# Optimization experiments

Measured on AMD Instinct MI355X. Metric: run time of the kernel, lower is better.

## Reference

```python
import jax, jax.numpy as jnp
import numpy as np

D_MODEL, D_STATE, V_RANGE, IMG, K = 64, 16, 1, 32, 3
GROUPS = 4
EPS = 1e-5


def _gather_indices():
    H = W = IMG
    v_list = [(x, y) for x in range(-V_RANGE, V_RANGE + 1) for y in range(-V_RANGE, V_RANGE + 1)]
    idx = []
    yg, xg = np.meshgrid(np.arange(H), np.arange(W), indexing='ij')
    for vx, vy in v_list:
        src_y = (yg - vy) % H
        src_x = (xg - vx) % W
        idx.append((src_y * W + src_x).reshape(-1))
    return jnp.asarray(np.stack(idx, axis=0), dtype=jnp.int32)  # (V, H*W)


def setup_inputs() -> dict:
    key = jax.random.key(0)
    ks = jax.random.split(key, 8)
    B = 4
    V = (2 * V_RANGE + 1) ** 2
    fan = D_MODEL * K * K
    std = 1.0 / np.sqrt(fan)
    return {
        'u_t': jax.random.normal(ks[0], (B, D_MODEL, IMG, IMG), jnp.float32),
        's_prev': jax.random.normal(ks[1], (B, V, D_MODEL, D_STATE, IMG, IMG), jnp.float32),
        'gamma': jnp.ones((D_MODEL,), jnp.float32),
        'beta': jnp.zeros((D_MODEL,), jnp.float32),
        'w_delta': jax.random.uniform(ks[2], (D_MODEL, D_MODEL, K, K), jnp.float32, -std, std),
        'b_delta': jax.random.uniform(ks[3], (D_MODEL,), jnp.float32, -std, std),
        'w_B': jax.random.uniform(ks[4], (D_STATE, D_MODEL, K, K), jnp.float32, -std, std),
        'w_C': jax.random.uniform(ks[5], (D_STATE, D_MODEL, K, K), jnp.float32, -std, std),
        'log_A_real': jnp.log(0.5 * jnp.ones((D_MODEL, D_STATE), jnp.float32)),
        'D_param': jnp.ones((D_MODEL,), jnp.float32),
        'dt_inv_softplus': jnp.asarray(np.log(np.exp(1.0) - 1.0), jnp.float32),
        'gather_indices': _gather_indices(),
    }


def _group_norm(x, gamma, beta):
    B, D, H, W = x.shape
    xg = x.reshape(B, GROUPS, D // GROUPS, H, W)
    mu = xg.mean(axis=(2, 3, 4), keepdims=True)
    var = xg.var(axis=(2, 3, 4), keepdims=True)
    xn = ((xg - mu) / jnp.sqrt(var + EPS)).reshape(B, D, H, W)
    return xn * gamma[None, :, None, None] + beta[None, :, None, None]


def _circ_conv(x, w, b=None):
    p = K // 2
    xp = jnp.pad(x, ((0, 0), (0, 0), (p, p), (p, p)), mode='wrap')
    y = jax.lax.conv_general_dilated(xp, w, (1, 1), 'VALID',
                                     dimension_numbers=('NCHW', 'OIHW', 'NCHW'))
    if b is not None:
        y = y + b[None, :, None, None]
    return y


def reference(u_t, s_prev, gamma, beta, w_delta, b_delta, w_B, w_C,
              log_A_real, D_param, dt_inv_softplus, gather_indices):
    B, D, H, W = u_t.shape
    Bv, V, _, N, _, _ = s_prev.shape
    u_norm = _group_norm(u_t, gamma, beta)
    delta = jax.nn.softplus(_circ_conv(u_norm, w_delta, b_delta) + dt_inv_softplus)
    delta = jnp.clip(delta, 1e-4, 5.0)                      # (B,D,H,W)
    B_val = _circ_conv(u_norm, w_B)                          # (B,N,H,W)
    C_val = _circ_conv(u_norm, w_C)                          # (B,N,H,W)
    A = -jnp.exp(log_A_real)                                 # (D,N)
    A_bar = jnp.exp(delta[:, :, None] * A[None, :, :, None, None])  # (B,D,N,H,W)
    B_bar = delta[:, :, None] * B_val[:, None]               # (B,D,N,H,W)
    # flow transport: per-velocity periodic-shift gather over flattened HW
    s_flat = s_prev.reshape(B, V, D, N, H * W)
    s_trans = jax.vmap(lambda sv, iv: jnp.take(sv, iv, axis=-1),
                       in_axes=(1, 0), out_axes=1)(s_flat, gather_indices)
    s_trans = s_trans.reshape(B, V, D, N, H, W)
    s_new = A_bar[:, None] * s_trans + B_bar[:, None] * u_t[:, None, :, None]
    y_state = jnp.sum(s_new * C_val[:, None, None], axis=3)  # (B,V,D,H,W)
    y_new = y_state + u_t[:, None] * D_param[None, None, :, None, None]
    return (y_new, s_new)
```

## Files before the change

kernel.cpp:

```cpp
#include <hip/hip_runtime.h>
#include <hip/hip_bf16.h>

#define D_MODEL 64
#define D_STATE 16
#define IMG     32
#define HW      (IMG*IMG)
#define V       9
#define B       4
#define GROUPS  4
#define CPG     (D_MODEL/GROUPS)

typedef float f32x4 __attribute__((ext_vector_type(4)));

__global__ __launch_bounds__(256) void gn_kernel(
    const float* __restrict__ u, const float* __restrict__ gamma,
    const float* __restrict__ beta, float* __restrict__ un)
{
    const int b = blockIdx.x / GROUPS;
    const int g = blockIdx.x % GROUPS;
    const float* base = u + ((size_t)b*D_MODEL + g*CPG) * HW;
    const int NE = CPG * HW;

    float s = 0.f, s2 = 0.f;
    for (int i = threadIdx.x; i < NE; i += 256) {
        float v = base[i];
        s += v; s2 += v*v;
    }
    for (int off = 32; off; off >>= 1) {
        s  += __shfl_down(s,  off);
        s2 += __shfl_down(s2, off);
    }
    __shared__ float red0[4], red1[4];
    const int wave = threadIdx.x >> 6;
    if ((threadIdx.x & 63) == 0) { red0[wave] = s; red1[wave] = s2; }
    __syncthreads();
    if (threadIdx.x == 0) {
        float a = 0.f, c = 0.f;
        for (int i = 0; i < 4; i++) { a += red0[i]; c += red1[i]; }
        red0[0] = a; red1[0] = c;
    }
    __syncthreads();
    const float mean = red0[0] * (1.f/16384.f);
    const float var  = red1[0] * (1.f/16384.f) - mean*mean;
    const float rstd = rsqrtf(var + 1e-5f);

    for (int i = threadIdx.x; i < NE; i += 256) {
        int c = i >> 10;
        int d = g*CPG + c;
        float v = (base[i] - mean) * rstd;
        un[((size_t)b*D_MODEL + d)*HW + (i & (HW-1))] = v*gamma[d] + beta[d];
    }
}

__global__ __launch_bounds__(256) void conv_kernel(
    const float* __restrict__ un,
    const float* __restrict__ w_delta, const float* __restrict__ b_delta,
    const float* __restrict__ w_B, const float* __restrict__ w_C,
    const float* __restrict__ dt_sp,
    float* __restrict__ delta, float* __restrict__ Bv, float* __restrict__ Cv)
{
    const int bx    = blockIdx.x;
    const int strip = bx & 3;
    const int cog   = (bx >> 2) % 24;
    const int b     = bx / 96;
    const int co0   = cog * 4;
    const int row0  = strip * 8;

    __shared__ float xs[16][10][32];
    __shared__ float wl[4][D_MODEL*9];

    for (int i = threadIdx.x; i < 4*D_MODEL*9; i += 256) {
        const int cl = i / (D_MODEL*9);
        const int rest = i % (D_MODEL*9);
        const int co = co0 + cl;
        const float* w = (co < 64) ? (w_delta + (size_t)co*(D_MODEL*9))
                       : (co < 80) ? (w_B + (size_t)(co-64)*(D_MODEL*9))
                                   : (w_C + (size_t)(co-80)*(D_MODEL*9));
        wl[cl][rest] = w[rest];
    }

    const int ly = threadIdx.x >> 5;
    const int ox = threadIdx.x & 31;
    const int oy = row0 + ly;

    const float* x = un + (size_t)b*D_MODEL*HW;
    float a0 = 0.f, a1 = 0.f, a2 = 0.f, a3 = 0.f;

    for (int c = 0; c < 4; c++) {
        __syncthreads();
        for (int i = threadIdx.x; i < 16*10*32; i += 256) {
            const int ci = i / 320;
            const int rr = (i % 320) >> 5;
            const int xx = i & 31;
            const int gy = (row0 - 1 + rr) & 31;
            xs[ci][rr][xx] = x[(size_t)(c*16 + ci)*HW + (gy << 5) + xx];
        }
        __syncthreads();

        #pragma unroll
        for (int ci = 0; ci < 16; ci++) {
            float v[3][3];
            #pragma unroll
            for (int dy = 0; dy < 3; dy++)
                #pragma unroll
                for (int dx = 0; dx < 3; dx++)
                    v[dy][dx] = xs[ci][ly + dy][(ox + dx + 31) & 31];
            const int cig = c*16 + ci;
            const float* w0 = &wl[0][cig*9];
            const float* w1 = &wl[1][cig*9];
            const float* w2 = &wl[2][cig*9];
            const float* w3 = &wl[3][cig*9];
            #pragma unroll
            for (int t = 0; t < 9; t++) {
                const float xv = v[t/3][t%3];
                a0 = fmaf(xv, w0[t], a0);
                a1 = fmaf(xv, w1[t], a1);
                a2 = fmaf(xv, w2[t], a2);
                a3 = fmaf(xv, w3[t], a3);
            }
        }
    }

    const int p = (oy << 5) + ox;
    const float dtsp = dt_sp[0];
    float accs[4] = {a0, a1, a2, a3};
    #pragma unroll
    for (int cl = 0; cl < 4; cl++) {
        const int co = co0 + cl;
        float acc = accs[cl];
        if (co < 64) {
            acc += b_delta[co] + dtsp;
            float sp = (acc > 15.f) ? acc : log1pf(__expf(acc));
            sp = fminf(fmaxf(sp, 1e-4f), 5.f);
            delta[((size_t)b*D_MODEL + co)*HW + p] = sp;
        } else if (co < 80) {
            Bv[((size_t)b*D_STATE + (co-64))*HW + p] = acc;
        } else {
            Cv[((size_t)b*D_STATE + (co-80))*HW + p] = acc;
        }
    }
}

__device__ __forceinline__ f32x4 asm_load4(const float* __restrict__ base, unsigned voff) {
    f32x4 d;
    asm volatile("global_load_dwordx4 %0, %1, %2"
                 : "=v"(d) : "v"(voff), "s"(base) : "memory");
    return d;
}

#define STEP(n, K) do { \
    if ((n) + 4 <= 15) { \
        sp[((n)+4)&15] = asm_load4(sp_u, sp_voff + ((n)+4)*4096u); \
        Bn[((n)+4)&15] = asm_load4(Bv_u, bc_voff + ((n)+4)*4096u); \
        Cn[((n)+4)&15] = asm_load4(Cv_u, bc_voff + ((n)+4)*4096u); \
    } \
    asm volatile("s_waitcnt vmcnt(" #K ")" ::: "memory"); \
    __builtin_amdgcn_sched_barrier(0); \
    { \
        const f32x4 own = sp[(n)]; \
        f32x4 s; \
        if (MODE == 0) { s = own; } \
        else if (MODE == 1) { const float nb = __shfl(own.x, laneR, 64); \
                              s.x = own.y; s.y = own.z; s.z = own.w; s.w = nb; } \
        else { const float nb = __shfl(own.w, laneL, 64); \
               s.x = nb; s.y = own.x; s.z = own.y; s.w = own.z; } \
        const float anr = an_[(n)]; \
        f32x4 ab; \
        ab.x = __expf(dl.x*anr); ab.y = __expf(dl.y*anr); \
        ab.z = __expf(dl.z*anr); ab.w = __expf(dl.w*anr); \
        const f32x4 snv = ab*s + du*Bn[(n)]; \
        __builtin_nontemporal_store(snv, (f32x4*)(sn_p + (n)*HW)); \
        y += snv * Cn[(n)]; \
    } \
} while (0)

template<int MODE>
__device__ __forceinline__ void pipe_body(
    const float* __restrict__ sp_u, unsigned sp_voff,
    const float* __restrict__ Bv_u, const float* __restrict__ Cv_u, unsigned bc_voff,
    float* __restrict__ sn_p,
    const f32x4 dl, const f32x4 du, const float* an_,
    f32x4& y, int laneL, int laneR)
{
    f32x4 sp[16], Bn[16], Cn[16];
    #pragma unroll
    for (int p = 0; p < 4; p++) {
        sp[p] = asm_load4(sp_u, sp_voff + p*4096u);
        Bn[p] = asm_load4(Bv_u, bc_voff + p*4096u);
        Cn[p] = asm_load4(Cv_u, bc_voff + p*4096u);
    }
    STEP(0, 12); STEP(1, 13); STEP(2, 14); STEP(3, 15);
    STEP(4, 16); STEP(5, 16); STEP(6, 16); STEP(7, 16);
    STEP(8, 16); STEP(9, 16); STEP(10, 16); STEP(11, 16);
    STEP(12, 13); STEP(13, 10); STEP(14, 7); STEP(15, 4);
}

__global__ __launch_bounds__(256) void main_kernel(
    const float* __restrict__ sprev, const float* __restrict__ ut,
    const float* __restrict__ delta, const float* __restrict__ Bv,
    const float* __restrict__ Cv, const float* __restrict__ logA,
    const float* __restrict__ Dp, const int* __restrict__ gidx,
    float* __restrict__ ynew, float* __restrict__ snew)
{
    const int blk = blockIdx.x;
    const int d   = blk % D_MODEL;
    const int tmp = blk / D_MODEL;
    const int v   = tmp % V;
    const int b   = tmp / V;

    const int t  = threadIdx.x;
    const int p0 = t * 4;
    const int y0 = p0 >> 5;
    const int x0 = p0 & 31;

    const int gi0 = gidx[v*HW];
    const int ryo = gi0 >> 5;
    const int rxo = gi0 & 31;

    const int ys   = (y0 + ryo) & 31;
    const int srcv = (ys << 5) + x0;

    const int lane  = t & 63;
    const int laneL = (lane & ~7) | ((lane + 7) & 7);
    const int laneR = (lane & ~7) | ((lane + 1) & 7);

    const size_t bvd = (((size_t)b*V + v)*D_MODEL + d);
    const float* sp_u = sprev + bvd * D_STATE * HW;
    float* sn_p = snew + bvd * D_STATE * HW + p0;

    const float dpd = Dp[d];
    float an_[D_STATE];
    #pragma unroll
    for (int n = 0; n < D_STATE; n++) an_[n] = -__expf(logA[d*D_STATE + n]);

    const f32x4 dl = *(const f32x4*)(delta + ((size_t)b*D_MODEL + d)*HW + p0);
    const f32x4 uu = *(const f32x4*)(ut    + ((size_t)b*D_MODEL + d)*HW + p0);
    const f32x4 du = dl * uu;
    const float* Bv_u = Bv + (size_t)b*D_STATE*HW;
    const float* Cv_u = Cv + (size_t)b*D_STATE*HW;

    f32x4 y = uu * dpd;

    const unsigned sp_voff = (unsigned)srcv * 4u;
    const unsigned bc_voff = (unsigned)p0 * 4u;

    if (rxo == 0) {
        pipe_body<0>(sp_u, sp_voff, Bv_u, Cv_u, bc_voff, sn_p, dl, du, an_, y, laneL, laneR);
    } else if (rxo == 1) {
        pipe_body<1>(sp_u, sp_voff, Bv_u, Cv_u, bc_voff, sn_p, dl, du, an_, y, laneL, laneR);
    } else if (rxo == 31) {
        pipe_body<2>(sp_u, sp_voff, Bv_u, Cv_u, bc_voff, sn_p, dl, du, an_, y, laneL, laneR);
    } else {
        const int4 src4 = *(const int4*)(gidx + v*HW + p0);
        #pragma unroll
        for (int n = 0; n < D_STATE; n++) {
            const float* sp_n = sp_u + n*HW;
            const f32x4 Bn = *(const f32x4*)(Bv_u + n*HW + p0);
            const f32x4 Cn = *(const f32x4*)(Cv_u + n*HW + p0);
            const float anr = an_[n];
            f32x4 s;
            s.x = sp_n[src4.x]; s.y = sp_n[src4.y];
            s.z = sp_n[src4.z]; s.w = sp_n[src4.w];
            f32x4 ab;
            ab.x = __expf(dl.x * anr);
            ab.y = __expf(dl.y * anr);
            ab.z = __expf(dl.z * anr);
            ab.w = __expf(dl.w * anr);
            const f32x4 sn = ab * s + du * Bn;
            __builtin_nontemporal_store(sn, (f32x4*)(sn_p + n*HW));
            y += sn * Cn;
        }
    }
    *(f32x4*)(ynew + bvd * HW + p0) = y;
}

extern "C" void kernel_launch(void* const* d_in, const int* in_sizes, int n_in,
                              void* d_out, int out_size, void* d_ws, size_t ws_size,
                              hipStream_t stream)
{
    const float* u_t       = (const float*)d_in[0];
    const float* s_prev    = (const float*)d_in[1];
    const float* gamma     = (const float*)d_in[2];
    const float* beta      = (const float*)d_in[3];
    const float* w_delta   = (const float*)d_in[4];
    const float* b_delta   = (const float*)d_in[5];
    const float* w_B       = (const float*)d_in[6];
    const float* w_C       = (const float*)d_in[7];
    const float* log_A     = (const float*)d_in[8];
    const float* D_param   = (const float*)d_in[9];
    const float* dt_sp     = (const float*)d_in[10];
    const int*   gidx      = (const int*)d_in[11];

    float* ws = (float*)d_ws;
    float* un    = ws;
    float* delta = un    + (size_t)B*D_MODEL*HW;
    float* Bv    = delta + (size_t)B*D_MODEL*HW;
    float* Cv    = Bv    + (size_t)B*D_STATE*HW;

    float* ynew = (float*)d_out;
    float* snew = ynew + (size_t)B*V*D_MODEL*HW;

    gn_kernel<<<B*GROUPS, 256, 0, stream>>>(u_t, gamma, beta, un);
    conv_kernel<<<B*96, 256, 0, stream>>>(un, w_delta, b_delta, w_B, w_C, dt_sp,
                                          delta, Bv, Cv);
    main_kernel<<<B*V*D_MODEL, 256, 0, stream>>>(s_prev, u_t, delta, Bv, Cv,
                                                 log_A, D_param, gidx, ynew, snew);
}
```

Baseline: 102.4 us.

## Restructure load pipeline: deeper prefetch, merged shift modes, deferred stores

Replaces the three templated pipelined bodies with one unified path that selects the shift mode at runtime, prefetches six states ahead with an 8-deep ring buffer, and folds the delta/u loads into the asm-counted load stream. All new-state results are buffered in registers and stored only after the loop, so loads no longer interleave with stores in the vmcnt accounting. The aim is a deeper memory pipeline and less instruction-cache footprint. In exchange it holds 16 extra vector registers for the deferred stores, always performs both shuffles, and relies on exact hand-counted vmcnt values.

Measured after the change: 102.2 us. About the same (-0.2%).

```diff
diff --git a/kernel.cpp b/kernel.cpp
--- a/kernel.cpp
+++ b/kernel.cpp
@@ -148,52 +148,28 @@
     return d;
 }
 
-#define STEP(n, K) do { \
-    if ((n) + 4 <= 15) { \
-        sp[((n)+4)&15] = asm_load4(sp_u, sp_voff + ((n)+4)*4096u); \
-        Bn[((n)+4)&15] = asm_load4(Bv_u, bc_voff + ((n)+4)*4096u); \
-        Cn[((n)+4)&15] = asm_load4(Cv_u, bc_voff + ((n)+4)*4096u); \
-    } \
-    asm volatile("s_waitcnt vmcnt(" #K ")" ::: "memory"); \
-    __builtin_amdgcn_sched_barrier(0); \
-    { \
-        const f32x4 own = sp[(n)]; \
-        f32x4 s; \
-        if (MODE == 0) { s = own; } \
-        else if (MODE == 1) { const float nb = __shfl(own.x, laneR, 64); \
-                              s.x = own.y; s.y = own.z; s.z = own.w; s.w = nb; } \
-        else { const float nb = __shfl(own.w, laneL, 64); \
-               s.x = nb; s.y = own.x; s.z = own.y; s.w = own.z; } \
-        const float anr = an_[(n)]; \
-        f32x4 ab; \
-        ab.x = __expf(dl.x*anr); ab.y = __expf(dl.y*anr); \
-        ab.z = __expf(dl.z*anr); ab.w = __expf(dl.w*anr); \
-        const f32x4 snv = ab*s + du*Bn[(n)]; \
-        __builtin_nontemporal_store(snv, (f32x4*)(sn_p + (n)*HW)); \
-        y += snv * Cn[(n)]; \
-    } \
-} while (0)
-
-template<int MODE>
-__device__ __forceinline__ void pipe_body(
-    const float* __restrict__ sp_u, unsigned sp_voff,
-    const float* __restrict__ Bv_u, const float* __restrict__ Cv_u, unsigned bc_voff,
-    float* __restrict__ sn_p,
-    const f32x4 dl, const f32x4 du, const float* an_,
-    f32x4& y, int laneL, int laneR)
-{
-    f32x4 sp[16], Bn[16], Cn[16];
-    #pragma unroll
-    for (int p = 0; p < 4; p++) {
-        sp[p] = asm_load4(sp_u, sp_voff + p*4096u);
-        Bn[p] = asm_load4(Bv_u, bc_voff + p*4096u);
-        Cn[p] = asm_load4(Cv_u, bc_voff + p*4096u);
-    }
-    STEP(0, 12); STEP(1, 13); STEP(2, 14); STEP(3, 15);
-    STEP(4, 16); STEP(5, 16); STEP(6, 16); STEP(7, 16);
-    STEP(8, 16); STEP(9, 16); STEP(10, 16); STEP(11, 16);
-    STEP(12, 13); STEP(13, 10); STEP(14, 7); STEP(15, 4);
-}
+#define WAITK(K) do { asm volatile("s_waitcnt vmcnt(%0)" :: "i"(K) : "memory"); \
+                      __builtin_amdgcn_sched_barrier(0); } while (0)
+
+#define LOADP(p) do { \
+    spr[(p)&7] = asm_load4(sp_u, sp_voff + (p)*4096u); \
+    Bnr[(p)&7] = asm_load4(Bv_u, bc_voff + (p)*4096u); \
+    Cnr[(p)&7] = asm_load4(Cv_u, bc_voff + (p)*4096u); } while (0)
+
+#define COMP(n) do { \
+    const f32x4 own = spr[(n)&7]; \
+    const float nbR = __shfl(own.x, laneR, 64); \
+    const float nbL = __shfl(own.w, laneL, 64); \
+    f32x4 s; \
+    if (rxo == 0)      { s = own; } \
+    else if (rxo == 1) { s.x = own.y; s.y = own.z; s.z = own.w; s.w = nbR; } \
+    else               { s.x = nbL; s.y = own.x; s.z = own.y; s.w = own.z; } \
+    const float anr = an_[(n)]; \
+    f32x4 ab; \
+    ab.x = __expf(dl.x*anr); ab.y = __expf(dl.y*anr); \
+    ab.z = __expf(dl.z*anr); ab.w = __expf(dl.w*anr); \
+    sn[(n)] = ab*s + du*Bnr[(n)&7]; \
+    y += sn[(n)] * Cnr[(n)&7]; } while (0)
 
 __global__ __launch_bounds__(256) void main_kernel(
     const float* __restrict__ sprev, const float* __restrict__ ut,
@@ -233,25 +209,52 @@
     #pragma unroll
     for (int n = 0; n < D_STATE; n++) an_[n] = -__expf(logA[d*D_STATE + n]);
 
-    const f32x4 dl = *(const f32x4*)(delta + ((size_t)b*D_MODEL + d)*HW + p0);
-    const f32x4 uu = *(const f32x4*)(ut    + ((size_t)b*D_MODEL + d)*HW + p0);
-    const f32x4 du = dl * uu;
+    const float* dl_u = delta + ((size_t)b*D_MODEL + d)*HW;
+    const float* u_u  = ut    + ((size_t)b*D_MODEL + d)*HW;
     const float* Bv_u = Bv + (size_t)b*D_STATE*HW;
     const float* Cv_u = Cv + (size_t)b*D_STATE*HW;
 
-    f32x4 y = uu * dpd;
-
     const unsigned sp_voff = (unsigned)srcv * 4u;
     const unsigned bc_voff = (unsigned)p0 * 4u;
-
-    if (rxo == 0) {
-        pipe_body<0>(sp_u, sp_voff, Bv_u, Cv_u, bc_voff, sn_p, dl, du, an_, y, laneL, laneR);
-    } else if (rxo == 1) {
-        pipe_body<1>(sp_u, sp_voff, Bv_u, Cv_u, bc_voff, sn_p, dl, du, an_, y, laneL, laneR);
-    } else if (rxo == 31) {
-        pipe_body<2>(sp_u, sp_voff, Bv_u, Cv_u, bc_voff, sn_p, dl, du, an_, y, laneL, laneR);
+    const unsigned uvoff   = (unsigned)p0 * 4u;
+
+    if (rxo == 0 || rxo == 1 || rxo == 31) {
+        f32x4 spr[8], Bnr[8], Cnr[8], sn[16];
+
+        f32x4 dl = asm_load4(dl_u, uvoff);
+        f32x4 uu = asm_load4(u_u,  uvoff);
+        LOADP(0); LOADP(1); LOADP(2); LOADP(3); LOADP(4); LOADP(5);
+        WAITK(18);
+        const f32x4 du = dl * uu;
+        f32x4 y = uu * dpd;
+
+        LOADP(6);  WAITK(18); COMP(0);
+        LOADP(7);  WAITK(18); COMP(1);
+        LOADP(8);  WAITK(18); COMP(2);
+        LOADP(9);  WAITK(18); COMP(3);
+        LOADP(10); WAITK(18); COMP(4);
+        LOADP(11); WAITK(18); COMP(5);
+        LOADP(12); WAITK(18); COMP(6);
+        LOADP(13); WAITK(18); COMP(7);
+        LOADP(14); WAITK(18); COMP(8);
+        LOADP(15); WAITK(18); COMP(9);
+        WAITK(15); COMP(10);
+        WAITK(12); COMP(11);
+        WAITK(9);  COMP(12);
+        WAITK(6);  COMP(13);
+        WAITK(3);  COMP(14);
+        WAITK(0);  COMP(15);
+
+        #pragma unroll
+        for (int n = 0; n < D_STATE; n++)
+            __builtin_nontemporal_store(sn[n], (f32x4*)(sn_p + n*HW));
+        *(f32x4*)(ynew + bvd * HW + p0) = y;
     } else {
         const int4 src4 = *(const int4*)(gidx + v*HW + p0);
+        const f32x4 dl = *(const f32x4*)(dl_u + p0);
+        const f32x4 uu = *(const f32x4*)(u_u + p0);
+        const f32x4 du = dl * uu;
+        f32x4 y = uu * dpd;
         #pragma unroll
         for (int n = 0; n < D_STATE; n++) {
             const float* sp_n = sp_u + n*HW;
@@ -266,12 +269,12 @@
             ab.y = __expf(dl.y * anr);
             ab.z = __expf(dl.z * anr);
             ab.w = __expf(dl.w * anr);
-            const f32x4 sn = ab * s + du * Bn;
-            __builtin_nontemporal_store(sn, (f32x4*)(sn_p + n*HW));
-            y += sn * Cn;
+            const f32x4 snv = ab * s + du * Bn;
+            __builtin_nontemporal_store(snv, (f32x4*)(sn_p + n*HW));
+            y += snv * Cn;
         }
-    }
-    *(f32x4*)(ynew + bvd * HW + p0) = y;
+        *(f32x4*)(ynew + bvd * HW + p0) = y;
+    }
 }
 
 extern "C" void kernel_launch(void* const* d_in, const int* in_sizes, int n_in,
```
